# Kernel optimization log

Measured on AMD Instinct MI355X. Metric: run time of the kernel, lower is better.

## Reference

```python
import jax, jax.numpy as jnp
import numpy as np

N = 100_000   # nodes
E = 1_600_000 # edges
G = 2_000     # graphs
P = 4_096     # ranking pairs
F_IN = 9      # num_node_features
U = 128       # model_units


def _linear_init(key, fan_in, fan_out):
    k1, k2 = jax.random.split(key)
    s = 1.0 / np.sqrt(fan_in)
    W = jax.random.uniform(k1, (fan_in, fan_out), jnp.float32, -s, s)
    b = jax.random.uniform(k2, (fan_out,), jnp.float32, -s, s)
    return W, b


def setup_inputs() -> dict:
    key = jax.random.key(0)
    ks = jax.random.split(key, 12)
    x = jax.random.normal(ks[0], (N, F_IN), jnp.float32)
    edge_index = jax.random.randint(ks[1], (2, E), 0, N, dtype=jnp.int32)
    # sorted, even node->graph assignment; every graph non-empty
    batch = (jnp.arange(N, dtype=jnp.int32) * G) // N
    idx_a = jax.random.randint(ks[2], (P,), 0, G, dtype=jnp.int32)
    idx_b = jax.random.randint(ks[3], (P,), 0, G, dtype=jnp.int32)
    W_in, b_in = _linear_init(ks[4], F_IN, U)
    W1, b1 = _linear_init(ks[5], U, U)
    W2, b2 = _linear_init(ks[6], U, U)
    Wf1, bf1 = _linear_init(ks[7], U, U)
    Wf2, bf2 = _linear_init(ks[8], U, 32)
    Wf3, bf3 = _linear_init(ks[9], 32, 1)
    return dict(x=x, edge_index=edge_index, batch=batch, idx_a=idx_a, idx_b=idx_b,
                W_in=W_in, b_in=b_in, W1=W1, b1=b1, W2=W2, b2=b2,
                Wf1=Wf1, bf1=bf1, Wf2=Wf2, bf2=bf2, Wf3=Wf3, bf3=bf3)


def reference(x, edge_index, batch, idx_a, idx_b,
              W_in, b_in, W1, b1, W2, b2, Wf1, bf1, Wf2, bf2, Wf3, bf3):
    src, dst = edge_index[0], edge_index[1]
    n = x.shape[0]
    # GCN symmetric norm with self-loops: deg counts in-edges + self-loop
    deg = jax.ops.segment_sum(jnp.ones(src.shape[0], jnp.float32), dst, num_segments=n) + 1.0
    dinv = jax.lax.rsqrt(deg)
    edge_norm = (dinv[src] * dinv[dst])[:, None]   # [E,1]
    self_norm = (dinv * dinv)[:, None]             # [N,1]

    def gcn(h, W, b):
        h = h @ W
        agg = jax.ops.segment_sum(h[src] * edge_norm, dst, num_segments=n)
        return agg + h * self_norm + b

    h = jnp.tanh(gcn(x, W_in, b_in))
    # dropout with training=False is identity
    h = jnp.tanh(gcn(h, W1, b1))
    h = jnp.tanh(gcn(h, W2, b2))
    h = jnp.tanh(h @ Wf1 + bf1)
    h = jnp.tanh(h @ Wf2 + bf2)
    h = h @ Wf3 + bf3  # [N,1]

    # global_mean_pool over graphs
    counts = jax.ops.segment_sum(jnp.ones(n, jnp.float32), batch, num_segments=G)
    util = jax.ops.segment_sum(h, batch, num_segments=G) / jnp.maximum(counts, 1.0)[:, None]  # [G,1]

    u = util[:, 0]
    out = jax.nn.sigmoid(u[idx_b] - u[idx_a])  # [P]
    return out, util
```

## Files before the change

### kernel.cpp

```cpp
#include <hip/hip_runtime.h>
#include <hip/hip_bf16.h>
#include <math.h>


#define U 128
#define LDA 136
#define WB 9
#define WSZ 512
#define NJ1 256

typedef __attribute__((ext_vector_type(8))) short bf16x8;
typedef __attribute__((ext_vector_type(4))) float f32x4;
typedef __attribute__((ext_vector_type(2))) float f32x2;

__device__ __forceinline__ unsigned short f2bf(float f) {
    unsigned u = __float_as_uint(f);
    unsigned r = (u + 0x7fffu + ((u >> 16) & 1u)) >> 16;
    return (unsigned short)r;
}
__device__ __forceinline__ unsigned char f2fp8(float v) {
    return (unsigned char)(__builtin_amdgcn_cvt_pk_fp8_f32(v, v, 0, false) & 0xff);
}

__global__ __launch_bounds__(256) void k_hist1(const int* __restrict__ dst,
                                               int* __restrict__ hist_g, int E, int nw) {
    __shared__ int h[256];
    int b = blockIdx.x;
    for (int i = threadIdx.x; i < nw; i += 256) h[i] = 0;
    __syncthreads();
    int ch = (E + NJ1 - 1) / NJ1;
    int e0 = b * ch, e1 = min(e0 + ch, E);
    for (int e = e0 + threadIdx.x; e < e1; e += 256)
        atomicAdd(&h[dst[e] >> WB], 1);
    __syncthreads();
    for (int w = threadIdx.x; w < nw; w += 256) hist_g[w * NJ1 + b] = h[w];
}

__global__ __launch_bounds__(256) void k_escan1(int* __restrict__ a,
                                                int* __restrict__ bsum, int n) {
    __shared__ int sc[256];
    int t = threadIdx.x, b = blockIdx.x;
    int base = b * 1024 + t * 4;
    int v[4];
    int s = 0;
    #pragma unroll
    for (int j = 0; j < 4; ++j) {
        int idx = base + j;
        int d = (idx < n) ? a[idx] : 0;
        v[j] = s;
        s += d;
    }
    sc[t] = s;
    __syncthreads();
    for (int off = 1; off < 256; off <<= 1) {
        int x = (t >= off) ? sc[t - off] : 0;
        __syncthreads();
        sc[t] += x;
        __syncthreads();
    }
    int excl = sc[t] - s;
    #pragma unroll
    for (int j = 0; j < 4; ++j) {
        int idx = base + j;
        if (idx < n) a[idx] = v[j] + excl;
    }
    if (t == 255) bsum[b] = sc[255];
}

__global__ __launch_bounds__(256) void k_escan2(int* __restrict__ a,
                                                const int* __restrict__ bsum,
                                                int nb, int n) {
    __shared__ int sc[256];
    int t = threadIdx.x;
    int v = (t < nb) ? bsum[t] : 0;
    sc[t] = v;
    __syncthreads();
    for (int off = 1; off < 256; off <<= 1) {
        int u = (t >= off) ? sc[t - off] : 0;
        __syncthreads();
        sc[t] += u;
        __syncthreads();
    }
    int myoff = (blockIdx.x > 0) ? (sc[blockIdx.x] - bsum[blockIdx.x]) : 0;
    int base = blockIdx.x * 1024;
    #pragma unroll
    for (int j = 0; j < 4; ++j) {
        int idx = base + t + j * 256;
        if (idx < n) a[idx] += myoff;
    }
}

__global__ __launch_bounds__(256) void k_bucket(const int* __restrict__ src,
                                                const int* __restrict__ dst,
                                                const int* __restrict__ hist_g,
                                                int2* __restrict__ eb, int E, int nw) {
    __shared__ int lcur[256];
    int b = blockIdx.x;
    for (int w = threadIdx.x; w < nw; w += 256) lcur[w] = hist_g[w * NJ1 + b];
    __syncthreads();
    int ch = (E + NJ1 - 1) / NJ1;
    int e0 = b * ch, e1 = min(e0 + ch, E);
    for (int e = e0 + threadIdx.x; e < e1; e += 256) {
        int d = dst[e];
        int pos = atomicAdd(&lcur[d >> WB], 1);
        eb[pos] = make_int2(src[e], d);
    }
}

__global__ __launch_bounds__(256) void k_deg2(const int2* __restrict__ eb,
                                              const int* __restrict__ hist_g,
                                              int* __restrict__ deg, int E, int nw, int N) {
    __shared__ int h[WSZ];
    int w = blockIdx.x;
    h[threadIdx.x] = 0;
    h[threadIdx.x + 256] = 0;
    __syncthreads();
    int s0 = hist_g[w * NJ1];
    int s1 = (w + 1 < nw) ? hist_g[(w + 1) * NJ1] : E;
    for (int i = s0 + threadIdx.x; i < s1; i += 256)
        atomicAdd(&h[eb[i].y & (WSZ - 1)], 1);
    __syncthreads();
    int base = w << WB;
    if (base + threadIdx.x < N) deg[base + threadIdx.x] = h[threadIdx.x];
    if (base + 256 + threadIdx.x < N) deg[base + 256 + threadIdx.x] = h[256 + threadIdx.x];
}

__global__ __launch_bounds__(256) void k_scan1(const int* __restrict__ deg,
                                               int* __restrict__ rowptr1,
                                               int* __restrict__ bsum, int N) {
    __shared__ int sc[256];
    int t = threadIdx.x, b = blockIdx.x;
    int base = b * 1024 + t * 4;
    int v[4];
    int s = 0;
    #pragma unroll
    for (int j = 0; j < 4; ++j) {
        int idx = base + j;
        int d = (idx < N) ? deg[idx] : 0;
        s += d;
        v[j] = s;
    }
    sc[t] = s;
    __syncthreads();
    for (int off = 1; off < 256; off <<= 1) {
        int x = (t >= off) ? sc[t - off] : 0;
        __syncthreads();
        sc[t] += x;
        __syncthreads();
    }
    int excl = sc[t] - s;
    #pragma unroll
    for (int j = 0; j < 4; ++j) {
        int idx = base + j;
        if (idx < N) rowptr1[idx] = v[j] + excl;
    }
    if (t == 255) bsum[b] = sc[255];
}

__global__ __launch_bounds__(256) void k_scan23(int* __restrict__ rowptr,
                                                const int* __restrict__ bsum,
                                                int nb, int N) {
    __shared__ int sc[256];
    __shared__ int bo[256];
    int t = threadIdx.x;
    int v = (t < nb) ? bsum[t] : 0;
    sc[t] = v;
    __syncthreads();
    for (int off = 1; off < 256; off <<= 1) {
        int u = (t >= off) ? sc[t - off] : 0;
        __syncthreads();
        sc[t] += u;
        __syncthreads();
    }
    bo[t] = sc[t] - v;
    __syncthreads();
    int i = blockIdx.x * 256 + t;
    if (i < N) rowptr[1 + i] += bo[i >> 10];
    if (i == 0) rowptr[0] = 0;
}

__global__ __launch_bounds__(256) void k_scatter2(const int2* __restrict__ eb,
                                                  const int* __restrict__ hist_g,
                                                  const int* __restrict__ rowptr,
                                                  int* __restrict__ csr_src,
                                                  int E, int nw, int N) {
    __shared__ int cur[WSZ];
    int w = blockIdx.x;
    int base = w << WB;
    int i0 = base + threadIdx.x, i1 = base + 256 + threadIdx.x;
    cur[threadIdx.x] = (i0 < N) ? rowptr[i0] : 0;
    cur[threadIdx.x + 256] = (i1 < N) ? rowptr[i1] : 0;
    __syncthreads();
    int s0 = hist_g[w * NJ1];
    int s1 = (w + 1 < nw) ? hist_g[(w + 1) * NJ1] : E;
    for (int i = s0 + threadIdx.x; i < s1; i += 256) {
        int2 e = eb[i];
        int pos = atomicAdd(&cur[e.y & (WSZ - 1)], 1);
        csr_src[pos] = e.x;
    }
}

__global__ __launch_bounds__(256) void k_prep(const int* __restrict__ deg,
                                              const float* __restrict__ x,
                                              const int* __restrict__ batch,
                                              const float* __restrict__ W1,
                                              const float* __restrict__ W2,
                                              const float* __restrict__ Wf1,
                                              const float* __restrict__ Wf2,
                                              float* __restrict__ dinv,
                                              float* __restrict__ xs,
                                              int* __restrict__ cnt,
                                              unsigned short* __restrict__ W1t,
                                              unsigned short* __restrict__ W2t,
                                              unsigned short* __restrict__ Wf1t,
                                              unsigned short* __restrict__ Wf2t, int N) {
    int t = blockIdx.x * 256 + threadIdx.x;
    if (t < N) {
        float dv = rsqrtf((float)deg[t] + 1.0f);
        dinv[t] = dv;
        #pragma unroll
        for (int k = 0; k < 9; ++k) xs[t * 16 + k] = x[t * 9 + k] * dv;
        #pragma unroll
        for (int k = 9; k < 16; ++k) xs[t * 16 + k] = 0.0f;
        atomicAdd(&cnt[batch[t]], 1);
    }
    if (t < 16384) {
        int n = t >> 7, k = t & 127;
        W1t[n * 128 + k] = f2bf(W1[k * 128 + n]);
        Wf1t[n * 128 + k] = f2bf(Wf1[k * 128 + n]);
    } else if (t < 32768) {
        int i = t - 16384, n = i >> 7, k = i & 127;
        W2t[n * 128 + k] = f2bf(W2[k * 128 + n]);
    } else if (t < 36864) {
        int i = t - 32768, n = i >> 7, k = i & 127;
        Wf2t[n * 128 + k] = f2bf(Wf2[k * 32 + n]);
    }
}

__global__ __launch_bounds__(256) void k_aggx(const float* __restrict__ xs,
                                              const int* __restrict__ rowptr,
                                              const int* __restrict__ csr_src,
                                              const float* __restrict__ dinv,
                                              float* __restrict__ xa, int N) {
    int node = blockIdx.x * 16 + (threadIdx.x >> 4);
    if (node >= N) return;
    int lane = threadIdx.x & 15;
    int s = rowptr[node], e = rowptr[node + 1];
    float a0 = 0.0f, a1 = 0.0f, a2 = 0.0f, a3 = 0.0f;
    int i = s;
    for (; i + 4 <= e; i += 4) {
        int s0 = csr_src[i], s1 = csr_src[i + 1];
        int s2 = csr_src[i + 2], s3 = csr_src[i + 3];
        a0 += xs[s0 * 16 + lane];
        a1 += xs[s1 * 16 + lane];
        a2 += xs[s2 * 16 + lane];
        a3 += xs[s3 * 16 + lane];
    }
    for (; i < e; ++i) {
        int s0 = csr_src[i];
        a0 += xs[s0 * 16 + lane];
    }
    if (lane < 9) {
        float dv = dinv[node];
        xa[node * 9 + lane] = dv * (a0 + a1 + a2 + a3 + xs[node * 16 + lane]);
    }
}

__global__ void k_gemm_in9(const float* __restrict__ xa, const float* __restrict__ Wi,
                           const float* __restrict__ bi, unsigned short* __restrict__ T,
                           int N) {
    int t = blockIdx.x * 256 + threadIdx.x;
    if (t < N * U) {
        int n = t >> 7, c = t & 127;
        const float* xr = xa + n * 9;
        float acc = bi[c];
        #pragma unroll
        for (int k = 0; k < 9; ++k) acc += xr[k] * Wi[k * U + c];
        T[t] = f2bf(tanhf(acc));
    }
}

__global__ __launch_bounds__(256) void k_gemm_mfma(const unsigned short* __restrict__ A,
                                                   const unsigned short* __restrict__ Wt,
                                                   const float* __restrict__ dinv,
                                                   unsigned char* __restrict__ Out, int N) {
    const int tid = threadIdx.x;
    const int wave = tid >> 6, lane = tid & 63;
    const int m16 = lane & 15, q = lane >> 4;
    const int row0 = blockIdx.x * 64 + wave * 16;
    int arow_idx = row0 + m16;
    if (arow_idx >= N) arow_idx = N - 1;
    const bf16x8* arow = (const bf16x8*)(A + (size_t)arow_idx * U + q * 8);
    f32x4 acc[8];
    #pragma unroll
    for (int t = 0; t < 8; ++t) acc[t] = (f32x4){0.f, 0.f, 0.f, 0.f};
    #pragma unroll
    for (int kc = 0; kc < 4; ++kc) {
        bf16x8 af = arow[kc * 4];
        #pragma unroll
        for (int t = 0; t < 8; ++t) {
            bf16x8 bfr = *(const bf16x8*)(Wt + ((t * 16 + m16) * 128 + kc * 32 + q * 8));
            acc[t] = __builtin_amdgcn_mfma_f32_16x16x32_bf16(af, bfr, acc[t], 0, 0, 0);
        }
    }
    float dv[4];
    #pragma unroll
    for (int r = 0; r < 4; ++r) {
        int gr = row0 + q * 4 + r;
        dv[r] = (gr < N) ? dinv[gr] : 0.0f;
    }
    #pragma unroll
    for (int t = 0; t < 8; ++t) {
        #pragma unroll
        for (int r = 0; r < 4; ++r) {
            int gr = row0 + q * 4 + r;
            if (gr < N) Out[(size_t)gr * U + t * 16 + m16] = f2fp8(acc[t][r] * dv[r]);
        }
    }
}

__global__ __launch_bounds__(256) void k_aggb(const unsigned char* __restrict__ Tb,
                                              const int* __restrict__ rowptr,
                                              const int* __restrict__ csr_src,
                                              const float* __restrict__ dinv,
                                              const float* __restrict__ bias,
                                              unsigned short* __restrict__ Out, int N) {
    int node = blockIdx.x * 4 + (threadIdx.x >> 6);
    if (node >= N) return;
    int lane = threadIdx.x & 63;
    const unsigned short* T16 = (const unsigned short*)Tb;
    float ax = 0.0f, ay = 0.0f, bx = 0.0f, by = 0.0f;
    int s = rowptr[node], e = rowptr[node + 1];
    int i = s;
    for (; i + 8 <= e; i += 8) {
        int idx[8];
        #pragma unroll
        for (int u = 0; u < 8; ++u) idx[u] = csr_src[i + u];
        unsigned uv[8];
        #pragma unroll
        for (int u = 0; u < 8; ++u) uv[u] = T16[idx[u] * 64 + lane];
        #pragma unroll
        for (int u = 0; u < 8; u += 2) {
            f32x2 f0 = __builtin_amdgcn_cvt_pk_f32_fp8(uv[u], false);
            f32x2 f1 = __builtin_amdgcn_cvt_pk_f32_fp8(uv[u + 1], false);
            ax += f0[0] + f1[0];
            ay += f0[1] + f1[1];
        }
    }
    for (; i + 4 <= e; i += 4) {
        int s0 = csr_src[i], s1 = csr_src[i + 1];
        int s2 = csr_src[i + 2], s3 = csr_src[i + 3];
        f32x2 f0 = __builtin_amdgcn_cvt_pk_f32_fp8((unsigned)T16[s0 * 64 + lane], false);
        f32x2 f1 = __builtin_amdgcn_cvt_pk_f32_fp8((unsigned)T16[s1 * 64 + lane], false);
        f32x2 f2 = __builtin_amdgcn_cvt_pk_f32_fp8((unsigned)T16[s2 * 64 + lane], false);
        f32x2 f3 = __builtin_amdgcn_cvt_pk_f32_fp8((unsigned)T16[s3 * 64 + lane], false);
        ax += f0[0] + f1[0];
        ay += f0[1] + f1[1];
        bx += f2[0] + f3[0];
        by += f2[1] + f3[1];
    }
    for (; i < e; ++i) {
        int s0 = csr_src[i];
        f32x2 f0 = __builtin_amdgcn_cvt_pk_f32_fp8((unsigned)T16[s0 * 64 + lane], false);
        ax += f0[0];
        ay += f0[1];
    }
    float dv = dinv[node];
    f32x2 fs = __builtin_amdgcn_cvt_pk_f32_fp8((unsigned)T16[node * 64 + lane], false);
    float2 bb = *(const float2*)&bias[lane * 2];
    float ox = tanhf(dv * (ax + bx + fs[0]) + bb.x);
    float oy = tanhf(dv * (ay + by + fs[1]) + bb.y);
    unsigned o = (unsigned)f2bf(ox) | ((unsigned)f2bf(oy) << 16);
    ((unsigned*)Out)[node * 64 + lane] = o;
}

__global__ __launch_bounds__(256, 2) void k_mlp(const unsigned short* __restrict__ H,
                                                const unsigned short* __restrict__ Wf1t,
                                                const float* __restrict__ bf1,
                                                const unsigned short* __restrict__ Wf2t,
                                                const float* __restrict__ bf2,
                                                const float* __restrict__ Wf3,
                                                const float* __restrict__ bf3,
                                                const int* __restrict__ batch,
                                                float* __restrict__ util_sum,
                                                int N, int G) {
    __shared__ unsigned short H2[4][16 * LDA];
    __shared__ float gsum[8];
    const int tid = threadIdx.x;
    if (tid < 8) gsum[tid] = 0.0f;
    const int wave = tid >> 6, lane = tid & 63;
    const int m16 = lane & 15, q = lane >> 4;
    const int blk0 = blockIdx.x * 256;
    const int g0 = batch[min(blk0, N - 1)];
    bf16x8 w1[4][8], w2[4][2];
    #pragma unroll
    for (int kc = 0; kc < 4; ++kc) {
        #pragma unroll
        for (int t = 0; t < 8; ++t)
            w1[kc][t] = *(const bf16x8*)(Wf1t + ((t * 16 + m16) * 128 + kc * 32 + q * 8));
        #pragma unroll
        for (int t = 0; t < 2; ++t)
            w2[kc][t] = *(const bf16x8*)(Wf2t + ((t * 16 + m16) * 128 + kc * 32 + q * 8));
    }
    float b1v[8];
    #pragma unroll
    for (int t = 0; t < 8; ++t) b1v[t] = bf1[t * 16 + m16];
    const float b2lo = bf2[m16], b2hi = bf2[m16 + 16];
    const float w3lo = Wf3[m16], w3hi = Wf3[m16 + 16];
    const float bf3v = bf3[0];
    __syncthreads();
    unsigned short* h2s = H2[wave];
    const int wbase = blk0 + wave * 64;
    bf16x8 a[4];
    {
        int ar = wbase + m16;
        if (ar >= N) ar = N - 1;
        const bf16x8* arow = (const bf16x8*)(H + (size_t)ar * U + q * 8);
        #pragma unroll
        for (int kc = 0; kc < 4; ++kc) a[kc] = arow[kc * 4];
    }
    for (int tile = 0; tile < 4; ++tile) {
        const int row0 = wbase + tile * 16;
        bf16x8 an[4];
        if (tile < 3) {
            int ar = row0 + 16 + m16;
            if (ar >= N) ar = N - 1;
            const bf16x8* arow = (const bf16x8*)(H + (size_t)ar * U + q * 8);
            #pragma unroll
            for (int kc = 0; kc < 4; ++kc) an[kc] = arow[kc * 4];
        }
        f32x4 acc[8];
        #pragma unroll
        for (int t = 0; t < 8; ++t) acc[t] = (f32x4){0.f, 0.f, 0.f, 0.f};
        #pragma unroll
        for (int kc = 0; kc < 4; ++kc) {
            #pragma unroll
            for (int t = 0; t < 8; ++t)
                acc[t] = __builtin_amdgcn_mfma_f32_16x16x32_bf16(a[kc], w1[kc][t], acc[t], 0, 0, 0);
        }
        #pragma unroll
        for (int t = 0; t < 8; ++t) {
            #pragma unroll
            for (int r = 0; r < 4; ++r) {
                int lr = q * 4 + r;
                h2s[lr * LDA + t * 16 + m16] = f2bf(tanhf(acc[t][r] + b1v[t]));
            }
        }
        f32x4 acc2[2];
        acc2[0] = (f32x4){0.f, 0.f, 0.f, 0.f};
        acc2[1] = (f32x4){0.f, 0.f, 0.f, 0.f};
        const unsigned short* h2row = h2s + m16 * LDA + q * 8;
        #pragma unroll
        for (int kc = 0; kc < 4; ++kc) {
            bf16x8 af = *(const bf16x8*)(h2row + kc * 32);
            #pragma unroll
            for (int t = 0; t < 2; ++t)
                acc2[t] = __builtin_amdgcn_mfma_f32_16x16x32_bf16(af, w2[kc][t], acc2[t], 0, 0, 0);
        }
        #pragma unroll
        for (int r = 0; r < 4; ++r) {
            float t0 = tanhf(acc2[0][r] + b2lo);
            float t1 = tanhf(acc2[1][r] + b2hi);
            float v = t0 * w3lo + t1 * w3hi;
            v += __shfl_xor(v, 1);
            v += __shfl_xor(v, 2);
            v += __shfl_xor(v, 4);
            v += __shfl_xor(v, 8);
            if (m16 == 0) {
                int n = row0 + q * 4 + r;
                if (n < N) atomicAdd(&gsum[batch[n] - g0], v + bf3v);
            }
        }
        #pragma unroll
        for (int kc = 0; kc < 4; ++kc) a[kc] = an[kc];
    }
    __syncthreads();
    if (tid < 8) {
        int g = g0 + tid;
        if (g < G) {
            float s = gsum[tid];
            if (s != 0.0f) atomicAdd(&util_sum[g], s);
        }
    }
}

__global__ void k_out(const float* __restrict__ us, const int* __restrict__ cnt,
                      const int* __restrict__ ia, const int* __restrict__ ib,
                      float* __restrict__ out, int P, int G) {
    int t = blockIdx.x * 256 + threadIdx.x;
    if (t < G) out[P + t] = us[t] / fmaxf((float)cnt[t], 1.0f);
    if (t < P) {
        int a = ia[t], b = ib[t];
        float ua = us[a] / fmaxf((float)cnt[a], 1.0f);
        float ub = us[b] / fmaxf((float)cnt[b], 1.0f);
        out[t] = 1.0f / (1.0f + expf(-(ub - ua)));
    }
}

extern "C" void kernel_launch(void* const* d_in, const int* in_sizes, int n_in,
                              void* d_out, int out_size, void* d_ws, size_t ws_size,
                              hipStream_t stream) {
    const float* x     = (const float*)d_in[0];
    const int*   eidx  = (const int*)d_in[1];
    const int*   batch = (const int*)d_in[2];
    const int*   idx_a = (const int*)d_in[3];
    const int*   idx_b = (const int*)d_in[4];
    const float* W_in  = (const float*)d_in[5];
    const float* b_in  = (const float*)d_in[6];
    const float* W1    = (const float*)d_in[7];
    const float* b1    = (const float*)d_in[8];
    const float* W2    = (const float*)d_in[9];
    const float* b2    = (const float*)d_in[10];
    const float* Wf1   = (const float*)d_in[11];
    const float* bf1   = (const float*)d_in[12];
    const float* Wf2   = (const float*)d_in[13];
    const float* bf2   = (const float*)d_in[14];
    const float* Wf3   = (const float*)d_in[15];
    const float* bf3   = (const float*)d_in[16];
    float* out = (float*)d_out;

    const int N = in_sizes[0] / 9;
    const int E = in_sizes[1] / 2;
    const int P = in_sizes[3];
    const int G = out_size - P;

    const int* src = eidx;
    const int* dst = eidx + E;

    const int nw = (N + WSZ - 1) >> WB;
    const int nb = (N + 1023) / 1024;
    const int nh = nw * NJ1;
    const int nbh = (nh + 1023) / 1024;

    char* ws = (char*)d_ws;
    size_t off = 0;
    auto take = [&](size_t bytes) -> void* {
        void* p = ws + off;
        off = (off + bytes + 255) & ~(size_t)255;
        return p;
    };
    int*   deg      = (int*)  take((size_t)N * 4);
    float* dinv     = (float*)take((size_t)N * 4);
    int*   rowptr   = (int*)  take((size_t)(N + 1) * 4);
    int*   bsum     = (int*)  take(256 * 4);
    int*   bsum2    = (int*)  take(256 * 4);
    int*   hist_g   = (int*)  take((size_t)nh * 4);
    int2*  eb       = (int2*) take((size_t)E * 8);
    int*   csr_src  = (int*)  take((size_t)E * 4);
    float* xs       = (float*)take((size_t)N * 16 * 4);
    float* xa       = (float*)take((size_t)N * 9 * 4);
    unsigned short* bufA = (unsigned short*)take((size_t)N * U * 2);
    unsigned char*  Tb   = (unsigned char*) take((size_t)N * U);
    unsigned short* W1t  = (unsigned short*)take(128 * 128 * 2);
    unsigned short* W2t  = (unsigned short*)take(128 * 128 * 2);
    unsigned short* Wf1t = (unsigned short*)take(128 * 128 * 2);
    unsigned short* Wf2t = (unsigned short*)take(32 * 128 * 2);
    float* util_sum = (float*)take((size_t)G * 4 + (size_t)G * 4);
    int*   cnt      = (int*)(util_sum + G);
    (void)ws_size;

    hipMemsetAsync(util_sum, 0, (size_t)G * 8, stream);

    k_hist1<<<NJ1, 256, 0, stream>>>(dst, hist_g, E, nw);
    k_escan1<<<nbh, 256, 0, stream>>>(hist_g, bsum2, nh);
    k_escan2<<<nbh, 256, 0, stream>>>(hist_g, bsum2, nbh, nh);
    k_bucket<<<NJ1, 256, 0, stream>>>(src, dst, hist_g, eb, E, nw);
    k_deg2<<<nw, 256, 0, stream>>>(eb, hist_g, deg, E, nw, N);
    k_prep<<<(N + 255) / 256, 256, 0, stream>>>(deg, x, batch, W1, W2, Wf1, Wf2,
                                                dinv, xs, cnt, W1t, W2t, Wf1t, Wf2t, N);
    k_scan1<<<nb, 256, 0, stream>>>(deg, rowptr + 1, bsum, N);
    k_scan23<<<(N + 255) / 256, 256, 0, stream>>>(rowptr, bsum, nb, N);
    k_scatter2<<<nw, 256, 0, stream>>>(eb, hist_g, rowptr, csr_src, E, nw, N);

    const int aggGrid  = (N + 3) / 4;
    const int gemmGrid = (N + 63) / 64;

    k_aggx<<<(N + 15) / 16, 256, 0, stream>>>(xs, rowptr, csr_src, dinv, xa, N);
    k_gemm_in9<<<((size_t)N * U + 255) / 256, 256, 0, stream>>>(xa, W_in, b_in, bufA, N);

    k_gemm_mfma<<<gemmGrid, 256, 0, stream>>>(bufA, W1t, dinv, Tb, N);
    k_aggb<<<aggGrid, 256, 0, stream>>>(Tb, rowptr, csr_src, dinv, b1, bufA, N);
    k_gemm_mfma<<<gemmGrid, 256, 0, stream>>>(bufA, W2t, dinv, Tb, N);
    k_aggb<<<aggGrid, 256, 0, stream>>>(Tb, rowptr, csr_src, dinv, b2, bufA, N);

    k_mlp<<<(N + 255) / 256, 256, 0, stream>>>(bufA, Wf1t, bf1, Wf2t, bf2, Wf3, bf3,
                                               batch, util_sum, N, G);

    int mx = (P > G ? P : G);
    k_out<<<(mx + 255) / 256, 256, 0, stream>>>(util_sum, cnt, idx_a, idx_b, out, P, G);
}
```

Measured before the change: 458.7 us.

## Split wavefront into four edge-parallel groups in GCN gather kernels

The aggregation kernels now have each wavefront process four neighbor edges at once. Each 16-lane group loads a full 128-byte fp8 row as 8-byte vectors, and the partial sums are combined with cross-lane shuffles. The aggx kernel moves from 16 nodes per block to 4 nodes per block with the same four-group split. This is meant to raise memory-level parallelism and use wider loads per gathered row, at the cost of more accumulator registers, shuffle reductions and masked tail handling.

```diff
diff --git a/kernel.cpp b/kernel.cpp
--- a/kernel.cpp
+++ b/kernel.cpp
@@ -242,27 +242,38 @@
                                               const int* __restrict__ csr_src,
                                               const float* __restrict__ dinv,
                                               float* __restrict__ xa, int N) {
-    int node = blockIdx.x * 16 + (threadIdx.x >> 4);
+    int node = blockIdx.x * 4 + (threadIdx.x >> 6);
     if (node >= N) return;
-    int lane = threadIdx.x & 15;
+    int lane = threadIdx.x & 63;
+    int q = lane >> 4, l16 = lane & 15;
+    float a = 0.0f;
     int s = rowptr[node], e = rowptr[node + 1];
-    float a0 = 0.0f, a1 = 0.0f, a2 = 0.0f, a3 = 0.0f;
     int i = s;
+    for (; i + 16 <= e; i += 16) {
+        int idx[4];
+        #pragma unroll
+        for (int g = 0; g < 4; ++g) idx[g] = csr_src[i + g * 4 + q];
+        float v[4];
+        #pragma unroll
+        for (int g = 0; g < 4; ++g) v[g] = xs[(size_t)idx[g] * 16 + l16];
+        a += (v[0] + v[1]) + (v[2] + v[3]);
+    }
     for (; i + 4 <= e; i += 4) {
-        int s0 = csr_src[i], s1 = csr_src[i + 1];
-        int s2 = csr_src[i + 2], s3 = csr_src[i + 3];
-        a0 += xs[s0 * 16 + lane];
-        a1 += xs[s1 * 16 + lane];
-        a2 += xs[s2 * 16 + lane];
-        a3 += xs[s3 * 16 + lane];
-    }
-    for (; i < e; ++i) {
-        int s0 = csr_src[i];
-        a0 += xs[s0 * 16 + lane];
-    }
+        int idx = csr_src[i + q];
+        a += xs[(size_t)idx * 16 + l16];
+    }
+    int t = e - i;
+    if (t > 0) {
+        int ii = i + q;
+        if (ii >= e) ii = e - 1;
+        float m = (q < t) ? 1.0f : 0.0f;
+        a += m * xs[(size_t)csr_src[ii] * 16 + l16];
+    }
+    a += __shfl_xor(a, 16);
+    a += __shfl_xor(a, 32);
     if (lane < 9) {
         float dv = dinv[node];
-        xa[node * 9 + lane] = dv * (a0 + a1 + a2 + a3 + xs[node * 16 + lane]);
+        xa[node * 9 + lane] = dv * (a + xs[node * 16 + lane]);
     }
 }
 
@@ -328,50 +339,67 @@
     int node = blockIdx.x * 4 + (threadIdx.x >> 6);
     if (node >= N) return;
     int lane = threadIdx.x & 63;
-    const unsigned short* T16 = (const unsigned short*)Tb;
-    float ax = 0.0f, ay = 0.0f, bx = 0.0f, by = 0.0f;
+    int q = lane >> 4, l16 = lane & 15;
+    const uint2* T8 = (const uint2*)Tb;
+    float a[8] = {0.f, 0.f, 0.f, 0.f, 0.f, 0.f, 0.f, 0.f};
     int s = rowptr[node], e = rowptr[node + 1];
     int i = s;
-    for (; i + 8 <= e; i += 8) {
-        int idx[8];
-        #pragma unroll
-        for (int u = 0; u < 8; ++u) idx[u] = csr_src[i + u];
-        unsigned uv[8];
-        #pragma unroll
-        for (int u = 0; u < 8; ++u) uv[u] = T16[idx[u] * 64 + lane];
-        #pragma unroll
-        for (int u = 0; u < 8; u += 2) {
-            f32x2 f0 = __builtin_amdgcn_cvt_pk_f32_fp8(uv[u], false);
-            f32x2 f1 = __builtin_amdgcn_cvt_pk_f32_fp8(uv[u + 1], false);
-            ax += f0[0] + f1[0];
-            ay += f0[1] + f1[1];
+    for (; i + 16 <= e; i += 16) {
+        int idx[4];
+        #pragma unroll
+        for (int g = 0; g < 4; ++g) idx[g] = csr_src[i + g * 4 + q];
+        uint2 u[4];
+        #pragma unroll
+        for (int g = 0; g < 4; ++g) u[g] = T8[(size_t)idx[g] * 16 + l16];
+        #pragma unroll
+        for (int g = 0; g < 4; ++g) {
+            f32x2 f0 = __builtin_amdgcn_cvt_pk_f32_fp8(u[g].x, false);
+            f32x2 f1 = __builtin_amdgcn_cvt_pk_f32_fp8(u[g].x, true);
+            f32x2 f2 = __builtin_amdgcn_cvt_pk_f32_fp8(u[g].y, false);
+            f32x2 f3 = __builtin_amdgcn_cvt_pk_f32_fp8(u[g].y, true);
+            a[0] += f0[0]; a[1] += f0[1]; a[2] += f1[0]; a[3] += f1[1];
+            a[4] += f2[0]; a[5] += f2[1]; a[6] += f3[0]; a[7] += f3[1];
         }
     }
     for (; i + 4 <= e; i += 4) {
-        int s0 = csr_src[i], s1 = csr_src[i + 1];
-        int s2 = csr_src[i + 2], s3 = csr_src[i + 3];
-        f32x2 f0 = __builtin_amdgcn_cvt_pk_f32_fp8((unsigned)T16[s0 * 64 + lane], false);
-        f32x2 f1 = __builtin_amdgcn_cvt_pk_f32_fp8((unsigned)T16[s1 * 64 + lane], false);
-        f32x2 f2 = __builtin_amdgcn_cvt_pk_f32_fp8((unsigned)T16[s2 * 64 + lane], false);
-        f32x2 f3 = __builtin_amdgcn_cvt_pk_f32_fp8((unsigned)T16[s3 * 64 + lane], false);
-        ax += f0[0] + f1[0];
-        ay += f0[1] + f1[1];
-        bx += f2[0] + f3[0];
-        by += f2[1] + f3[1];
-    }
-    for (; i < e; ++i) {
-        int s0 = csr_src[i];
-        f32x2 f0 = __builtin_amdgcn_cvt_pk_f32_fp8((unsigned)T16[s0 * 64 + lane], false);
-        ax += f0[0];
-        ay += f0[1];
-    }
+        int idx = csr_src[i + q];
+        uint2 u = T8[(size_t)idx * 16 + l16];
+        f32x2 f0 = __builtin_amdgcn_cvt_pk_f32_fp8(u.x, false);
+        f32x2 f1 = __builtin_amdgcn_cvt_pk_f32_fp8(u.x, true);
+        f32x2 f2 = __builtin_amdgcn_cvt_pk_f32_fp8(u.y, false);
+        f32x2 f3 = __builtin_amdgcn_cvt_pk_f32_fp8(u.y, true);
+        a[0] += f0[0]; a[1] += f0[1]; a[2] += f1[0]; a[3] += f1[1];
+        a[4] += f2[0]; a[5] += f2[1]; a[6] += f3[0]; a[7] += f3[1];
+    }
+    int t = e - i;
+    if (t > 0) {
+        int ii = i + q;
+        if (ii >= e) ii = e - 1;
+        int idx = csr_src[ii];
+        uint2 u = T8[(size_t)idx * 16 + l16];
+        float m = (q < t) ? 1.0f : 0.0f;
+        f32x2 f0 = __builtin_amdgcn_cvt_pk_f32_fp8(u.x, false);
+        f32x2 f1 = __builtin_amdgcn_cvt_pk_f32_fp8(u.x, true);
+        f32x2 f2 = __builtin_amdgcn_cvt_pk_f32_fp8(u.y, false);
+        f32x2 f3 = __builtin_amdgcn_cvt_pk_f32_fp8(u.y, true);
+        a[0] += m * f0[0]; a[1] += m * f0[1]; a[2] += m * f1[0]; a[3] += m * f1[1];
+        a[4] += m * f2[0]; a[5] += m * f2[1]; a[6] += m * f3[0]; a[7] += m * f3[1];
+    }
+    #pragma unroll
+    for (int j = 0; j < 8; ++j) {
+        a[j] += __shfl_xor(a[j], 16);
+        a[j] += __shfl_xor(a[j], 32);
+    }
+    float sx = (q < 2) ? ((q == 0) ? a[0] : a[2]) : ((q == 2) ? a[4] : a[6]);
+    float sy = (q < 2) ? ((q == 0) ? a[1] : a[3]) : ((q == 2) ? a[5] : a[7]);
+    int f = 8 * l16 + 2 * q;
     float dv = dinv[node];
-    f32x2 fs = __builtin_amdgcn_cvt_pk_f32_fp8((unsigned)T16[node * 64 + lane], false);
-    float2 bb = *(const float2*)&bias[lane * 2];
-    float ox = tanhf(dv * (ax + bx + fs[0]) + bb.x);
-    float oy = tanhf(dv * (ay + by + fs[1]) + bb.y);
-    unsigned o = (unsigned)f2bf(ox) | ((unsigned)f2bf(oy) << 16);
-    ((unsigned*)Out)[node * 64 + lane] = o;
+    unsigned short selfu = *(const unsigned short*)(Tb + (size_t)node * 128 + f);
+    f32x2 fs = __builtin_amdgcn_cvt_pk_f32_fp8((unsigned)selfu, false);
+    float2 bb = *(const float2*)&bias[f];
+    float ox = tanhf(dv * (sx + fs[0]) + bb.x);
+    float oy = tanhf(dv * (sy + fs[1]) + bb.y);
+    ((unsigned*)Out)[node * 64 + (f >> 1)] = (unsigned)f2bf(ox) | ((unsigned)f2bf(oy) << 16);
 }
 
 __global__ __launch_bounds__(256, 2) void k_mlp(const unsigned short* __restrict__ H,
@@ -575,7 +603,7 @@
     const int aggGrid  = (N + 3) / 4;
     const int gemmGrid = (N + 63) / 64;
 
-    k_aggx<<<(N + 15) / 16, 256, 0, stream>>>(xs, rowptr, csr_src, dinv, xa, N);
+    k_aggx<<<aggGrid, 256, 0, stream>>>(xs, rowptr, csr_src, dinv, xa, N);
     k_gemm_in9<<<((size_t)N * U + 255) / 256, 256, 0, stream>>>(xa, W_in, b_in, bufA, N);
 
     k_gemm_mfma<<<gemmGrid, 256, 0, stream>>>(bufA, W1t, dinv, Tb, N);
```

Result: no change. 462.5 us (+0.8%).
